# Optimization experiments

Measured on AMD Instinct MI355X. Metric: run time of the kernel, lower is better.

## Reference

```python
import jax, jax.numpy as jnp
import numpy as np

IN_FEATURES = 4096
OUT_FEATURES = 4096
ALPHA = 0.002
BETA = 0.01


def setup_inputs() -> dict:
    key = jax.random.key(0)
    k_x, k_w, k_b = jax.random.split(key, 3)
    # int8 activations, weights, bias (matching torch.randint(-127, 127, ...))
    x = jax.random.randint(k_x, (4, 2048, IN_FEATURES), -127, 127, dtype=jnp.int32).astype(jnp.int8)
    weight = jax.random.randint(k_w, (OUT_FEATURES, IN_FEATURES), -127, 127, dtype=jnp.int32).astype(jnp.int8)
    bias = jax.random.randint(k_b, (1, OUT_FEATURES), -127, 127, dtype=jnp.int32).astype(jnp.int8)
    a = jnp.float32(ALPHA)
    b = jnp.float32(BETA)
    return {"x": x, "weight": weight, "bias": bias, "a": a, "b": b}


def reference(x, weight, bias, a, b):
    # int8 bias add, and requantize-to-int8 epilogue.
    x_shape = x.shape
    x2d = x.reshape(-1, x_shape[-1])                       # [M, K] int8
    # int32 accumulation: acc = x @ W^T
    acc = jnp.matmul(x2d.astype(jnp.int32), weight.T.astype(jnp.int32),
                     preferred_element_type=jnp.int32)      # [M, N] int32
    # epilogue: alpha * acc + beta * bias, round + clamp to int8 range
    y = a * acc.astype(jnp.float32) + b * bias.astype(jnp.float32)
    y = jnp.clip(jnp.round(y), -128.0, 127.0).astype(jnp.int8)
    return y.reshape(*x_shape[:-1], -1)
```

## Files before the change

kernel.cpp:

```cpp
#include <hip/hip_runtime.h>

#define K_DIM 4096
#define N_DIM 4096
#define NT (K_DIM / 64)

typedef int v4i __attribute__((ext_vector_type(4)));

__device__ __forceinline__ void gload_lds16(const void* g, void* l) {
  __builtin_amdgcn_global_load_lds(
      (const __attribute__((address_space(1))) void*)g,
      (__attribute__((address_space(3))) void*)l, 16, 0, 0);
}

__device__ __forceinline__ int pack4(int4 w) {
  return (w.x & 0xff) | ((w.y & 0xff) << 8) | ((w.z & 0xff) << 16) | (w.w << 24);
}

__global__ __launch_bounds__(256) void pack_kernel(const int* __restrict__ src,
                                                   int4* __restrict__ dst, int n16) {
  int i = blockIdx.x * 256 + threadIdx.x;
  if (i >= n16) return;
  const int4* s = (const int4*)src + (size_t)i * 4;
  int4 w0 = s[0], w1 = s[1], w2 = s[2], w3 = s[3];
  int4 r;
  r.x = pack4(w0); r.y = pack4(w1); r.z = pack4(w2); r.w = pack4(w3);
  dst[i] = r;
}

__global__ __launch_bounds__(512, 2) void gemm256(
    const char* __restrict__ Ap, const char* __restrict__ Bp,
    const int* __restrict__ bias, const float* __restrict__ pa,
    const float* __restrict__ pb, int* __restrict__ out) {
  extern __shared__ __align__(16) char lds[];

  const int tid = threadIdx.x;
  const int wid = tid >> 6;
  const int lane = tid & 63;

  const int nwg = gridDim.x;
  const int cpx = nwg >> 3;
  const int flat = blockIdx.x;
  const int wg = (flat & 7) * cpx + (flat >> 3);
  const int br = wg >> 4;
  const int bn = wg & 15;

  const int wr = wid >> 2;
  const int wcol = wid & 3;

  const int srow = tid >> 2;
  const int schunk = (tid & 3) ^ ((tid >> 3) & 3);
  const char* aSrc = Ap + (size_t)(br * 256 + srow) * K_DIM + schunk * 16;
  const char* bSrc = Bp + (size_t)(bn * 256 + srow) * K_DIM + schunk * 16;
  char* const ldsA = lds;
  char* const ldsB = lds + 65536;

  auto stageA = [&](int kt) {
    const char* s = aSrc + kt * 64;
    char* d = ldsA + (kt & 3) * 16384 + wid * 1024;
    gload_lds16(s, d);
    gload_lds16(s + (size_t)128 * K_DIM, d + 8192);
  };
  auto stageB = [&](int kt) {
    const char* s = bSrc + kt * 64;
    char* d = ldsB + (kt & 3) * 16384 + wid * 1024;
    gload_lds16(s, d);
    gload_lds16(s + (size_t)128 * K_DIM, d + 8192);
  };

  const int lrow = lane & 15;
  const int fchunk = lane >> 4;
  const int rchunk = fchunk ^ ((lrow >> 1) & 3);
  const int aOff = (wr * 128 + lrow) * 64 + rchunk * 16;
  const int bOff = 65536 + (wcol * 64 + lrow) * 64 + rchunk * 16;

  v4i acc[8][4];
  {
    v4i z = {0, 0, 0, 0};
#pragma unroll
    for (int mi = 0; mi < 8; ++mi)
#pragma unroll
      for (int ni = 0; ni < 4; ++ni) acc[mi][ni] = z;
  }

  stageA(0); stageB(0);
  stageA(1); stageB(1);
  stageA(2); stageB(2);

  for (int kt = 0; kt < NT; ++kt) {
    if (kt < NT - 2)
      asm volatile("s_waitcnt vmcnt(8)" ::: "memory");
    else if (kt == NT - 2)
      asm volatile("s_waitcnt vmcnt(4)" ::: "memory");
    else
      asm volatile("s_waitcnt vmcnt(0)" ::: "memory");
    __builtin_amdgcn_s_barrier();

    const int sb = (kt & 3) * 16384;

    v4i af[4], bf[4];
#pragma unroll
    for (int mi = 0; mi < 4; ++mi) af[mi] = *(const v4i*)&lds[sb + aOff + mi * 1024];
#pragma unroll
    for (int ni = 0; ni < 4; ++ni) bf[ni] = *(const v4i*)&lds[sb + bOff + ni * 1024];
    if (kt < NT - 3) stageA(kt + 3);
    __builtin_amdgcn_s_barrier();
    __builtin_amdgcn_s_setprio(1);
#pragma unroll
    for (int mi = 0; mi < 4; ++mi)
#pragma unroll
      for (int ni = 0; ni < 4; ++ni)
        acc[mi][ni] =
            __builtin_amdgcn_mfma_i32_16x16x64_i8(af[mi], bf[ni], acc[mi][ni], 0, 0, 0);
    __builtin_amdgcn_s_setprio(0);

    v4i af2[4];
#pragma unroll
    for (int mi = 0; mi < 4; ++mi) af2[mi] = *(const v4i*)&lds[sb + aOff + (mi + 4) * 1024];
    if (kt < NT - 3) stageB(kt + 3);
    __builtin_amdgcn_s_barrier();
    __builtin_amdgcn_s_setprio(1);
#pragma unroll
    for (int mi = 0; mi < 4; ++mi)
#pragma unroll
      for (int ni = 0; ni < 4; ++ni)
        acc[mi + 4][ni] =
            __builtin_amdgcn_mfma_i32_16x16x64_i8(af2[mi], bf[ni], acc[mi + 4][ni], 0, 0, 0);
    __builtin_amdgcn_s_setprio(0);
  }

  const float alpha = *pa;
  const float beta = *pb;
  const int col = lane & 15;
  const int rg = lane >> 4;
#pragma unroll
  for (int ni = 0; ni < 4; ++ni) {
    const int n = bn * 256 + wcol * 64 + ni * 16 + col;
    const float bb = __fmul_rn(beta, (float)bias[n]);
#pragma unroll
    for (int mi = 0; mi < 8; ++mi) {
#pragma unroll
      for (int j = 0; j < 4; ++j) {
        const int m = br * 256 + wr * 128 + mi * 16 + rg * 4 + j;
        float y = __fadd_rn(__fmul_rn(alpha, (float)acc[mi][ni][j]), bb);
        y = rintf(y);
        y = fminf(127.f, fmaxf(-128.f, y));
        out[(size_t)m * N_DIM + n] = (int)y;
      }
    }
  }
}

extern "C" void kernel_launch(void* const* d_in, const int* in_sizes, int n_in,
                              void* d_out, int out_size, void* d_ws, size_t ws_size,
                              hipStream_t stream) {
  const int* x = (const int*)d_in[0];
  const int* w = (const int*)d_in[1];
  const int* bias = (const int*)d_in[2];
  const float* pa = (const float*)d_in[3];
  const float* pb = (const float*)d_in[4];
  int* out = (int*)d_out;

  const int M = in_sizes[0] / K_DIM;
  const size_t xBytes = (size_t)M * K_DIM;
  const size_t wBytes = (size_t)N_DIM * K_DIM;

  char* xp = (char*)d_ws;
  char* wp = xp + xBytes;
  const int n16x = (int)(xBytes / 16);
  const int n16w = (int)(wBytes / 16);
  pack_kernel<<<(n16x + 255) / 256, 256, 0, stream>>>(x, (int4*)xp, n16x);
  pack_kernel<<<(n16w + 255) / 256, 256, 0, stream>>>(w, (int4*)wp, n16w);

  const int nwg = (M / 256) * (N_DIM / 256);
  hipFuncSetAttribute((const void*)gemm256,
                      hipFuncAttributeMaxDynamicSharedMemorySize, 131072);
  gemm256<<<nwg, 512, 131072, stream>>>(xp, wp, bias, pa, pb, out);
}
```

Measured before the change: 196.9 us.

## Switch to 32x32x32 int8 MFMA with single-barrier pipelined k-loop

Replaces the 16x16x64 int8 MFMA tiling with 32x32x32 MFMAs, so each wave holds a 4x2 grid of 32x32 accumulator tiles instead of 8x4 of 16x16. This changes the LDS fragment-read pattern to two k-halves per tile and reworks the epilogue row mapping. The main loop is restructured to issue all A and B stage loads together, use lgkmcnt waits to overlap LDS reads with MFMA, and use one barrier per iteration instead of three. The aim is fewer LDS reads per MFMA and less synchronization. The risks are different register pressure and possible LDS bank conflicts from the new access pattern.

```diff
diff --git a/kernel.cpp b/kernel.cpp
--- a/kernel.cpp
+++ b/kernel.cpp
@@ -5,6 +5,7 @@
 #define NT (K_DIM / 64)
 
 typedef int v4i __attribute__((ext_vector_type(4)));
+typedef int v16i __attribute__((ext_vector_type(16)));
 
 __device__ __forceinline__ void gload_lds16(const void* g, void* l) {
   __builtin_amdgcn_global_load_lds(
@@ -51,97 +52,96 @@
   const int schunk = (tid & 3) ^ ((tid >> 3) & 3);
   const char* aSrc = Ap + (size_t)(br * 256 + srow) * K_DIM + schunk * 16;
   const char* bSrc = Bp + (size_t)(bn * 256 + srow) * K_DIM + schunk * 16;
-  char* const ldsA = lds;
-  char* const ldsB = lds + 65536;
 
-  auto stageA = [&](int kt) {
-    const char* s = aSrc + kt * 64;
-    char* d = ldsA + (kt & 3) * 16384 + wid * 1024;
-    gload_lds16(s, d);
-    gload_lds16(s + (size_t)128 * K_DIM, d + 8192);
-  };
-  auto stageB = [&](int kt) {
-    const char* s = bSrc + kt * 64;
-    char* d = ldsB + (kt & 3) * 16384 + wid * 1024;
-    gload_lds16(s, d);
-    gload_lds16(s + (size_t)128 * K_DIM, d + 8192);
+  auto stage = [&](int kt) {
+    const char* sa = aSrc + kt * 64;
+    const char* sb2 = bSrc + kt * 64;
+    char* da = lds + (kt & 3) * 16384 + wid * 1024;
+    char* db = lds + 65536 + (kt & 3) * 16384 + wid * 1024;
+    gload_lds16(sa, da);
+    gload_lds16(sa + (size_t)128 * K_DIM, da + 8192);
+    gload_lds16(sb2, db);
+    gload_lds16(sb2 + (size_t)128 * K_DIM, db + 8192);
   };
 
-  const int lrow = lane & 15;
-  const int fchunk = lane >> 4;
-  const int rchunk = fchunk ^ ((lrow >> 1) & 3);
-  const int aOff = (wr * 128 + lrow) * 64 + rchunk * 16;
-  const int bOff = 65536 + (wcol * 64 + lrow) * 64 + rchunk * 16;
+  const int lrow = lane & 31;
+  const int hi = lane >> 5;
+  const int swz = (lrow >> 1) & 3;
+  const int kOff0 = (hi ^ swz) << 4;
+  const int kOff1 = kOff0 ^ 32;
+  const int aBase = (wr * 128 + lrow) * 64;
+  const int bBase = 65536 + (wcol * 64 + lrow) * 64;
 
-  v4i acc[8][4];
+  v16i acc[4][2];
   {
-    v4i z = {0, 0, 0, 0};
+    v16i z = {0};
 #pragma unroll
-    for (int mi = 0; mi < 8; ++mi)
+    for (int mi = 0; mi < 4; ++mi)
 #pragma unroll
-      for (int ni = 0; ni < 4; ++ni) acc[mi][ni] = z;
+      for (int ni = 0; ni < 2; ++ni) acc[mi][ni] = z;
   }
 
-  stageA(0); stageB(0);
-  stageA(1); stageB(1);
-  stageA(2); stageB(2);
+  stage(0); stage(1); stage(2);
+  asm volatile("s_waitcnt vmcnt(8)" ::: "memory");
+  __builtin_amdgcn_s_barrier();
 
   for (int kt = 0; kt < NT; ++kt) {
-    if (kt < NT - 2)
-      asm volatile("s_waitcnt vmcnt(8)" ::: "memory");
-    else if (kt == NT - 2)
+    const int sb = (kt & 3) * 16384;
+
+    v4i a0[4], b0[2], a1[4], b1[2];
+#pragma unroll
+    for (int mi = 0; mi < 4; ++mi) a0[mi] = *(const v4i*)&lds[sb + aBase + mi * 2048 + kOff0];
+#pragma unroll
+    for (int ni = 0; ni < 2; ++ni) b0[ni] = *(const v4i*)&lds[sb + bBase + ni * 2048 + kOff0];
+#pragma unroll
+    for (int mi = 0; mi < 4; ++mi) a1[mi] = *(const v4i*)&lds[sb + aBase + mi * 2048 + kOff1];
+#pragma unroll
+    for (int ni = 0; ni < 2; ++ni) b1[ni] = *(const v4i*)&lds[sb + bBase + ni * 2048 + kOff1];
+
+    if (kt + 3 < NT) stage(kt + 3);
+
+    asm volatile("s_waitcnt lgkmcnt(6)" ::: "memory");
+    __builtin_amdgcn_sched_barrier(0);
+    __builtin_amdgcn_s_setprio(1);
+#pragma unroll
+    for (int mi = 0; mi < 4; ++mi)
+#pragma unroll
+      for (int ni = 0; ni < 2; ++ni)
+        acc[mi][ni] =
+            __builtin_amdgcn_mfma_i32_32x32x32_i8(a0[mi], b0[ni], acc[mi][ni], 0, 0, 0);
+    __builtin_amdgcn_s_setprio(0);
+
+    asm volatile("s_waitcnt lgkmcnt(0)" ::: "memory");
+    __builtin_amdgcn_sched_barrier(0);
+    __builtin_amdgcn_s_setprio(1);
+#pragma unroll
+    for (int mi = 0; mi < 4; ++mi)
+#pragma unroll
+      for (int ni = 0; ni < 2; ++ni)
+        acc[mi][ni] =
+            __builtin_amdgcn_mfma_i32_32x32x32_i8(a1[mi], b1[ni], acc[mi][ni], 0, 0, 0);
+    __builtin_amdgcn_s_setprio(0);
+
+    if (kt < NT - 3)
       asm volatile("s_waitcnt vmcnt(4)" ::: "memory");
     else
       asm volatile("s_waitcnt vmcnt(0)" ::: "memory");
     __builtin_amdgcn_s_barrier();
-
-    const int sb = (kt & 3) * 16384;
-
-    v4i af[4], bf[4];
-#pragma unroll
-    for (int mi = 0; mi < 4; ++mi) af[mi] = *(const v4i*)&lds[sb + aOff + mi * 1024];
-#pragma unroll
-    for (int ni = 0; ni < 4; ++ni) bf[ni] = *(const v4i*)&lds[sb + bOff + ni * 1024];
-    if (kt < NT - 3) stageA(kt + 3);
-    __builtin_amdgcn_s_barrier();
-    __builtin_amdgcn_s_setprio(1);
-#pragma unroll
-    for (int mi = 0; mi < 4; ++mi)
-#pragma unroll
-      for (int ni = 0; ni < 4; ++ni)
-        acc[mi][ni] =
-            __builtin_amdgcn_mfma_i32_16x16x64_i8(af[mi], bf[ni], acc[mi][ni], 0, 0, 0);
-    __builtin_amdgcn_s_setprio(0);
-
-    v4i af2[4];
-#pragma unroll
-    for (int mi = 0; mi < 4; ++mi) af2[mi] = *(const v4i*)&lds[sb + aOff + (mi + 4) * 1024];
-    if (kt < NT - 3) stageB(kt + 3);
-    __builtin_amdgcn_s_barrier();
-    __builtin_amdgcn_s_setprio(1);
-#pragma unroll
-    for (int mi = 0; mi < 4; ++mi)
-#pragma unroll
-      for (int ni = 0; ni < 4; ++ni)
-        acc[mi + 4][ni] =
-            __builtin_amdgcn_mfma_i32_16x16x64_i8(af2[mi], bf[ni], acc[mi + 4][ni], 0, 0, 0);
-    __builtin_amdgcn_s_setprio(0);
   }
 
   const float alpha = *pa;
   const float beta = *pb;
-  const int col = lane & 15;
-  const int rg = lane >> 4;
 #pragma unroll
-  for (int ni = 0; ni < 4; ++ni) {
-    const int n = bn * 256 + wcol * 64 + ni * 16 + col;
+  for (int ni = 0; ni < 2; ++ni) {
+    const int n = bn * 256 + wcol * 64 + ni * 32 + lrow;
     const float bb = __fmul_rn(beta, (float)bias[n]);
 #pragma unroll
-    for (int mi = 0; mi < 8; ++mi) {
+    for (int mi = 0; mi < 4; ++mi) {
 #pragma unroll
-      for (int j = 0; j < 4; ++j) {
-        const int m = br * 256 + wr * 128 + mi * 16 + rg * 4 + j;
-        float y = __fadd_rn(__fmul_rn(alpha, (float)acc[mi][ni][j]), bb);
+      for (int r = 0; r < 16; ++r) {
+        const int row = (r & 3) + 8 * (r >> 2) + 4 * hi;
+        const int m = br * 256 + wr * 128 + mi * 32 + row;
+        float y = __fadd_rn(__fmul_rn(alpha, (float)acc[mi][ni][r]), bb);
         y = rintf(y);
         y = fminf(127.f, fmaxf(-128.f, y));
         out[(size_t)m * N_DIM + n] = (int)y;
```

Measured after the change: 203.6 us. 1.03x slower.

## Restructure GEMM main loop to one barrier per k-step and merge pack launches

Applied to the files above, without the earlier changes.

The GEMM main loop now issues both A and B stage loads together and uses a single wait plus barrier at the end of each k-step, instead of two barriers per iteration. A fragments are software-pipelined two steps ahead, with sched_barriers interleaving the LDS reads between MFMA groups. The two int32-to-int8 pack kernels are merged into one launch covering both x and w, which removes one launch. The risk is more LDS-read latency exposure, a different overlap pattern that depends on the 4-slot ring buffer staying race-free, and extra register pressure from holding 8 A fragments.

```diff
diff --git a/kernel.cpp b/kernel.cpp
--- a/kernel.cpp
+++ b/kernel.cpp
@@ -16,11 +16,14 @@
   return (w.x & 0xff) | ((w.y & 0xff) << 8) | ((w.z & 0xff) << 16) | (w.w << 24);
 }
 
-__global__ __launch_bounds__(256) void pack_kernel(const int* __restrict__ src,
-                                                   int4* __restrict__ dst, int n16) {
+__global__ __launch_bounds__(256) void pack_kernel(const int* __restrict__ x,
+                                                   const int* __restrict__ w,
+                                                   int4* __restrict__ dst, int n16x,
+                                                   int n16) {
   int i = blockIdx.x * 256 + threadIdx.x;
   if (i >= n16) return;
-  const int4* s = (const int4*)src + (size_t)i * 4;
+  const int4* s = (i < n16x) ? ((const int4*)x + (size_t)i * 4)
+                             : ((const int4*)w + (size_t)(i - n16x) * 4);
   int4 w0 = s[0], w1 = s[1], w2 = s[2], w3 = s[3];
   int4 r;
   r.x = pack4(w0); r.y = pack4(w1); r.z = pack4(w2); r.w = pack4(w3);
@@ -51,20 +54,16 @@
   const int schunk = (tid & 3) ^ ((tid >> 3) & 3);
   const char* aSrc = Ap + (size_t)(br * 256 + srow) * K_DIM + schunk * 16;
   const char* bSrc = Bp + (size_t)(bn * 256 + srow) * K_DIM + schunk * 16;
-  char* const ldsA = lds;
-  char* const ldsB = lds + 65536;
 
-  auto stageA = [&](int kt) {
-    const char* s = aSrc + kt * 64;
-    char* d = ldsA + (kt & 3) * 16384 + wid * 1024;
-    gload_lds16(s, d);
-    gload_lds16(s + (size_t)128 * K_DIM, d + 8192);
-  };
-  auto stageB = [&](int kt) {
-    const char* s = bSrc + kt * 64;
-    char* d = ldsB + (kt & 3) * 16384 + wid * 1024;
-    gload_lds16(s, d);
-    gload_lds16(s + (size_t)128 * K_DIM, d + 8192);
+  auto stage = [&](int kt) {
+    const char* sa = aSrc + kt * 64;
+    const char* sb2 = bSrc + kt * 64;
+    char* da = lds + (kt & 3) * 16384 + wid * 1024;
+    char* db = lds + 65536 + (kt & 3) * 16384 + wid * 1024;
+    gload_lds16(sa, da);
+    gload_lds16(sa + (size_t)128 * K_DIM, da + 8192);
+    gload_lds16(sb2, db);
+    gload_lds16(sb2 + (size_t)128 * K_DIM, db + 8192);
   };
 
   const int lrow = lane & 15;
@@ -82,66 +81,54 @@
       for (int ni = 0; ni < 4; ++ni) acc[mi][ni] = z;
   }
 
-  stageA(0); stageB(0);
-  stageA(1); stageB(1);
-  stageA(2); stageB(2);
+  stage(0); stage(1); stage(2);
+  asm volatile("s_waitcnt vmcnt(8)" ::: "memory");
+  __builtin_amdgcn_s_barrier();
 
   for (int kt = 0; kt < NT; ++kt) {
-    if (kt < NT - 2)
-      asm volatile("s_waitcnt vmcnt(8)" ::: "memory");
-    else if (kt == NT - 2)
+    const int sb = (kt & 3) * 16384;
+
+    v4i bf[4], af[8];
+#pragma unroll
+    for (int ni = 0; ni < 4; ++ni) bf[ni] = *(const v4i*)&lds[sb + bOff + ni * 1024];
+    af[0] = *(const v4i*)&lds[sb + aOff + 0 * 1024];
+    af[1] = *(const v4i*)&lds[sb + aOff + 1 * 1024];
+    if (kt + 3 < NT) stage(kt + 3);
+    __builtin_amdgcn_sched_barrier(0);
+
+#pragma unroll
+    for (int mi = 0; mi < 8; ++mi) {
+      if (mi + 2 < 8) af[mi + 2] = *(const v4i*)&lds[sb + aOff + (mi + 2) * 1024];
+      __builtin_amdgcn_sched_barrier(0);
+      __builtin_amdgcn_s_setprio(1);
+#pragma unroll
+      for (int ni = 0; ni < 4; ++ni)
+        acc[mi][ni] =
+            __builtin_amdgcn_mfma_i32_16x16x64_i8(af[mi], bf[ni], acc[mi][ni], 0, 0, 0);
+      __builtin_amdgcn_s_setprio(0);
+      __builtin_amdgcn_sched_barrier(0);
+    }
+
+    if (kt < NT - 3)
       asm volatile("s_waitcnt vmcnt(4)" ::: "memory");
     else
       asm volatile("s_waitcnt vmcnt(0)" ::: "memory");
     __builtin_amdgcn_s_barrier();
-
-    const int sb = (kt & 3) * 16384;
-
-    v4i af[4], bf[4];
-#pragma unroll
-    for (int mi = 0; mi < 4; ++mi) af[mi] = *(const v4i*)&lds[sb + aOff + mi * 1024];
-#pragma unroll
-    for (int ni = 0; ni < 4; ++ni) bf[ni] = *(const v4i*)&lds[sb + bOff + ni * 1024];
-    if (kt < NT - 3) stageA(kt + 3);
-    __builtin_amdgcn_s_barrier();
-    __builtin_amdgcn_s_setprio(1);
-#pragma unroll
-    for (int mi = 0; mi < 4; ++mi)
-#pragma unroll
-      for (int ni = 0; ni < 4; ++ni)
-        acc[mi][ni] =
-            __builtin_amdgcn_mfma_i32_16x16x64_i8(af[mi], bf[ni], acc[mi][ni], 0, 0, 0);
-    __builtin_amdgcn_s_setprio(0);
-
-    v4i af2[4];
-#pragma unroll
-    for (int mi = 0; mi < 4; ++mi) af2[mi] = *(const v4i*)&lds[sb + aOff + (mi + 4) * 1024];
-    if (kt < NT - 3) stageB(kt + 3);
-    __builtin_amdgcn_s_barrier();
-    __builtin_amdgcn_s_setprio(1);
-#pragma unroll
-    for (int mi = 0; mi < 4; ++mi)
-#pragma unroll
-      for (int ni = 0; ni < 4; ++ni)
-        acc[mi + 4][ni] =
-            __builtin_amdgcn_mfma_i32_16x16x64_i8(af2[mi], bf[ni], acc[mi + 4][ni], 0, 0, 0);
-    __builtin_amdgcn_s_setprio(0);
   }
 
   const float alpha = *pa;
   const float beta = *pb;
-  const int col = lane & 15;
   const int rg = lane >> 4;
 #pragma unroll
   for (int ni = 0; ni < 4; ++ni) {
-    const int n = bn * 256 + wcol * 64 + ni * 16 + col;
-    const float bb = __fmul_rn(beta, (float)bias[n]);
+    const int n = bn * 256 + wcol * 64 + ni * 16 + lrow;
+    const float bb2 = __fmul_rn(beta, (float)bias[n]);
 #pragma unroll
     for (int mi = 0; mi < 8; ++mi) {
 #pragma unroll
       for (int j = 0; j < 4; ++j) {
         const int m = br * 256 + wr * 128 + mi * 16 + rg * 4 + j;
-        float y = __fadd_rn(__fmul_rn(alpha, (float)acc[mi][ni][j]), bb);
+        float y = __fadd_rn(__fmul_rn(alpha, (float)acc[mi][ni][j]), bb2);
         y = rintf(y);
         y = fminf(127.f, fmaxf(-128.f, y));
         out[(size_t)m * N_DIM + n] = (int)y;
@@ -167,9 +154,9 @@
   char* xp = (char*)d_ws;
   char* wp = xp + xBytes;
   const int n16x = (int)(xBytes / 16);
-  const int n16w = (int)(wBytes / 16);
-  pack_kernel<<<(n16x + 255) / 256, 256, 0, stream>>>(x, (int4*)xp, n16x);
-  pack_kernel<<<(n16w + 255) / 256, 256, 0, stream>>>(w, (int4*)wp, n16w);
+  const int n16 = (int)((xBytes + wBytes) / 16);
+  pack_kernel<<<(n16 + 255) / 256, 256, 0, stream>>>(x, (const int*)d_in[1],
+                                                     (int4*)xp, n16x, n16);
 
   const int nwg = (M / 256) * (N_DIM / 256);
   hipFuncSetAttribute((const void*)gemm256,
```

After: 195.0 us. Within noise of the previous version (-0.9%).
